# Kernel tuning notes

Measured on AMD Instinct MI355X. Metric: run time of the kernel, lower is better.

The kernel has to match this reference:

```python
import jax, jax.numpy as jnp
import numpy as np

N_NODES = 100000
N_EDGES = 800000
H = 128
MAX_Z = 1000
N_GRAPHS = 500  # batch = repeat(arange(500), 200); subgraphs are contiguous


def setup_inputs() -> dict:
    key = jax.random.key(0)
    ks = jax.random.split(key, 16)
    z = jax.random.randint(ks[0], (N_NODES,), 0, MAX_Z)
    edge_index = jax.random.randint(ks[1], (2, N_EDGES), 0, N_NODES)
    batch = jnp.repeat(jnp.arange(N_GRAPHS), N_NODES // N_GRAPHS)
    edge_mask = jax.random.randint(ks[2], (N_EDGES,), 0, 2).astype(bool)
    s = 1.0 / np.sqrt(H)
    inp = {
        "z": z, "edge_index": edge_index, "batch": batch, "edge_mask": edge_mask,
        "z_table": jax.random.normal(ks[3], (MAX_Z, H), dtype=jnp.float32) * 0.02,
        "W0": jax.random.uniform(ks[4], (H, H), minval=-s, maxval=s),
        "b0": jax.random.uniform(ks[5], (H,), minval=-s, maxval=s),
        "W1": jax.random.uniform(ks[6], (H, H), minval=-s, maxval=s),
        "b1": jax.random.uniform(ks[7], (H,), minval=-s, maxval=s),
        "W2": jax.random.uniform(ks[8], (H, H), minval=-s, maxval=s),
        "b2": jax.random.uniform(ks[9], (H,), minval=-s, maxval=s),
        "lin1_w": jax.random.uniform(ks[10], (H, H), minval=-s, maxval=s),
        "lin1_b": jax.random.uniform(ks[11], (H,), minval=-s, maxval=s),
        "lin2_w": jax.random.uniform(ks[12], (H, 1), minval=-s, maxval=s),
        "lin2_b": jax.random.uniform(ks[13], (1,), minval=-s, maxval=s),
    }
    return inp


def _gcn_conv(x, W, b, src, dst, w):
    # PyG GCNConv with self-loops (fill=1) and symmetric normalization.
    xw = x @ W                                                # [N,H]
    deg = jax.ops.segment_sum(w, dst, num_segments=N_NODES) + 1.0
    dinv = jax.lax.rsqrt(deg)                                 # deg >= 1 (self-loop)
    coef = (dinv[src] * w * dinv[dst])[:, None]               # [E,1]
    out = jax.ops.segment_sum(coef * xw[src], dst, num_segments=N_NODES)
    out = out + (dinv * dinv)[:, None] * xw                   # self-loop messages
    return out + b


def reference(z, edge_index, batch, edge_mask, z_table,
              W0, b0, W1, b1, W2, b2, lin1_w, lin1_b, lin2_w, lin2_b):
    x = z_table[z]                                            # z embedding, [N,H]
    src, dst = edge_index[0], edge_index[1]
    # fuse='minus': edge_index[:, edge_mask] == zero-weight masked-out edges
    w = edge_mask.astype(x.dtype)
    x = jax.nn.relu(_gcn_conv(x, W0, b0, src, dst, w))        # dropout: eval mode
    x = jax.nn.relu(_gcn_conv(x, W1, b1, src, dst, w))
    x = _gcn_conv(x, W2, b2, src, dst, w)
    # hadamard pooling: first two nodes of each (sorted, contiguous) subgraph
    center = jnp.searchsorted(batch, jnp.arange(N_GRAPHS))
    x = x[center] * x[center + 1]                             # [G,H]
    x = jax.nn.relu(x @ lin1_w + lin1_b)
    return x @ lin2_w + lin2_b                                # [G,1]
```

## Files before the change

kernel.cpp:

```cpp
#include <hip/hip_runtime.h>

#define N_NODES 100000
#define N_EDGES 800000
#define EHALF (N_EDGES / 2)
#define H 128
#define MAX_Z 1000
#define N_GRAPHS 500
#define ELL_CAP 32
#define NB 391
#define TB 125
#define MAXC1 33008
#define NC_ROWS 1008
#define CTR0 0
#define CTR1 64
#define LA_GRID 2080
#define LB_GRID 1040
#define N0_GRID 2064

typedef __attribute__((ext_vector_type(8))) short bf16x8;
typedef __attribute__((ext_vector_type(4))) float f32x4;

__device__ __forceinline__ unsigned short f2bf(float f) {
    union { float f; unsigned u; } x; x.f = f;
    unsigned r = x.u + 0x7fffu + ((x.u >> 16) & 1u);
    return (unsigned short)(r >> 16);
}
__device__ __forceinline__ float bf2f(unsigned short u) {
    return __uint_as_float((unsigned)u << 16);
}
__device__ __forceinline__ int clampid(int p) {
    return (p < 0 || p >= N_NODES) ? 0 : p;
}

__global__ void k_setup(int* fill, int* f0, int* f1, int* ctrs,
                        const float* W0, const float* W1, const float* W2,
                        unsigned short* Wp, const float* ztab,
                        unsigned short* tabb) {
    int b = blockIdx.x;
    if (b < NB) {
        int i = b * 256 + threadIdx.x;
        if (i < N_NODES) { fill[i] = 0; f0[i] = 0; f1[i] = 0; }
        if (i < 128) ctrs[i] = 0;
    } else if (b < NB + 24) {
        int bb = b - NB;
        int wi = bb >> 3;
        const float* W = (wi == 0) ? W0 : (wi == 1) ? W1 : W2;
        int t = (bb & 7) * 256 + threadIdx.x;
        int lane = t & 63, kt = (t >> 6) & 3, c = t >> 8;
        int quad = lane >> 4, n = c * 16 + (lane & 15);
        unsigned short o[8];
#pragma unroll
        for (int j = 0; j < 8; j++)
            o[j] = f2bf(W[(kt * 32 + quad * 8 + j) * H + n]);
        ushort4 lo = { o[0], o[1], o[2], o[3] }, hi = { o[4], o[5], o[6], o[7] };
        unsigned short* dst = Wp + (size_t)wi * 16384 + (size_t)t * 8;
        *(ushort4*)(dst)     = lo;
        *(ushort4*)(dst + 4) = hi;
    } else {
        int i = (b - NB - 24) * 256 + threadIdx.x;
        if (i < MAX_Z * H / 4) {
            float4 v = *(const float4*)(ztab + (size_t)i * 4);
            ushort4 o = { f2bf(v.x), f2bf(v.y), f2bf(v.z), f2bf(v.w) };
            *(ushort4*)(tabb + (size_t)i * 4) = o;
        }
    }
}

__global__ void k_edge(const int* __restrict__ src, const int* __restrict__ dst,
                       const int* __restrict__ mask, int* fill, int* ell) {
    int e = blockIdx.x * 256 + threadIdx.x;
    if (e >= EHALF) return;
    int m0 = mask[e], m1 = mask[e + EHALF];
    int d0 = dst[e],  d1 = dst[e + EHALF];
    int s0 = src[e],  s1 = src[e + EHALF];
    if (m0) {
        int p = atomicAdd(&fill[d0], 1);
        if (p < ELL_CAP) ell[(size_t)d0 * ELL_CAP + p] = s0;
    }
    if (m1) {
        int p = atomicAdd(&fill[d1], 1);
        if (p < ELL_CAP) ell[(size_t)d1 * ELL_CAP + p] = s1;
    }
}

__global__ void k_n1(const int* fill, const int* ell, int* f1, int* f0,
                     int* list1, int* list0, int* ctrs) {
    __shared__ int wtot[4];
    __shared__ int bbase0, bbase1;
    int tid = threadIdx.x, lane = tid & 63, wv = tid >> 6;
    int c = blockIdx.x * 4 + wv;
    int s = -1;
    if (c < 2 * N_GRAPHS) {
        int v = (c >> 1) * 200 + (c & 1);
        int n = fill[v]; if (n > ELL_CAP) n = ELL_CAP;
        s = (lane < n) ? ell[(size_t)v * ELL_CAP + lane] : ((lane == n) ? v : -1);
    }
    bool need = false;
    if (s >= 0 && atomicExch(&f1[s], 1) == 0) {
        f0[s] = 1;
        need = true;
    }
    unsigned long long b = __ballot(need);
    int total = __popcll(b);
    int pre = __popcll(b & ((1ull << lane) - 1ull));
    if (lane == 0) wtot[wv] = total;
    __syncthreads();
    if (tid == 0) {
        int bt = wtot[0] + wtot[1] + wtot[2] + wtot[3];
        if (bt) {
            bbase1 = atomicAdd(&ctrs[CTR1], bt);
            bbase0 = atomicAdd(&ctrs[CTR0], bt);
        }
    }
    __syncthreads();
    if (need) {
        int off = pre;
        for (int w2 = 0; w2 < 4; w2++) if (w2 < wv) off += wtot[w2];
        list1[bbase1 + off] = s;
        list0[bbase0 + off] = s;
    }
}

__global__ void k_n0(const int* fill, const int* ell, const int* list1,
                     int* f0, int* list0, int* ctrs) {
    __shared__ int wtot[4];
    __shared__ int bbase;
    int tid = threadIdx.x, lane = tid & 63, wv = tid >> 6;
    int cnt1 = ctrs[CTR1];
    for (int base = blockIdx.x * 4; base < cnt1; base += N0_GRID * 4) {
        int i = base + wv;
        bool need = false;
        int s = 0;
        if (i < cnt1) {
            int v = list1[i];
            int n = fill[v]; if (n > ELL_CAP) n = ELL_CAP;
            if (lane < n) {
                s = ell[(size_t)v * ELL_CAP + lane];
                need = (atomicExch(&f0[s], 1) == 0);
            }
        }
        unsigned long long b = __ballot(need);
        int total = __popcll(b);
        int pre = __popcll(b & ((1ull << lane) - 1ull));
        if (lane == 0) wtot[wv] = total;
        __syncthreads();
        if (tid == 0) {
            int bt = wtot[0] + wtot[1] + wtot[2] + wtot[3];
            if (bt) bbase = atomicAdd(&ctrs[CTR0], bt);
        }
        __syncthreads();
        if (need) {
            int off = pre;
            for (int w2 = 0; w2 < 4; w2++) if (w2 < wv) off += wtot[w2];
            list0[bbase + off] = s;
        }
        __syncthreads();
    }
}

__global__ __launch_bounds__(512) void k_layerA(const int* __restrict__ z,
                                                const unsigned short* __restrict__ tabb,
                                                const int* __restrict__ ell,
                                                const int* __restrict__ fill,
                                                const int* __restrict__ list,
                                                const int* countp,
                                                const unsigned short* __restrict__ Wp,
                                                const float* __restrict__ bias,
                                                unsigned short* xb) {
    __shared__ unsigned short yt[16][136];
    int count = *countp;
    int tid = threadIdx.x, lane = tid & 63, wv = tid >> 6;
    int l2 = lane * 2;
    int m = lane & 15, quad = lane >> 4;

    for (int t = blockIdx.x; t * 16 < count; t += LA_GRID) {
        for (int q = 0; q < 2; q++) {
            int r = t * 16 + wv * 2 + q;
            float ax = 0.f, ay = 0.f;
            if (r < count) {
                int v = list[r];
                int ntrue = fill[v];
                int px = 0;
                if (lane < ELL_CAP) px = ell[(size_t)v * ELL_CAP + lane];
                px = clampid(px);
                int zx = z[px];
                int fx = fill[px];
                int zv = z[v];
                int n = ntrue > ELL_CAP ? ELL_CAP : ntrue;
                float dv = rsqrtf(1.0f + (float)ntrue);
                float pc = (lane < n) ? rsqrtf(1.0f + (float)fx) * dv : 0.f;
                float sc = dv * dv;
                ushort2 xs = *(const ushort2*)(tabb + (size_t)zv * H + l2);
                ax = sc * bf2f(xs.x); ay = sc * bf2f(xs.y);
                int k = 0;
                for (; k + 3 < n; k += 4) {
                    int z0 = __shfl(zx, k),   z1 = __shfl(zx, k + 1);
                    int z2 = __shfl(zx, k + 2), z3 = __shfl(zx, k + 3);
                    float c0 = __shfl(pc, k),   c1 = __shfl(pc, k + 1);
                    float c2 = __shfl(pc, k + 2), c3 = __shfl(pc, k + 3);
                    ushort2 m0 = *(const ushort2*)(tabb + (size_t)z0 * H + l2);
                    ushort2 m1 = *(const ushort2*)(tabb + (size_t)z1 * H + l2);
                    ushort2 m2 = *(const ushort2*)(tabb + (size_t)z2 * H + l2);
                    ushort2 m3 = *(const ushort2*)(tabb + (size_t)z3 * H + l2);
                    ax += c0 * bf2f(m0.x) + c1 * bf2f(m1.x) + c2 * bf2f(m2.x) + c3 * bf2f(m3.x);
                    ay += c0 * bf2f(m0.y) + c1 * bf2f(m1.y) + c2 * bf2f(m2.y) + c3 * bf2f(m3.y);
                }
                for (; k < n; k++) {
                    int zz = __shfl(zx, k); float c = __shfl(pc, k);
                    ushort2 m0 = *(const ushort2*)(tabb + (size_t)zz * H + l2);
                    ax += c * bf2f(m0.x); ay += c * bf2f(m0.y);
                }
            }
            ushort2 o; o.x = f2bf(ax); o.y = f2bf(ay);
            *(ushort2*)&yt[wv * 2 + q][l2] = o;
        }
        __syncthreads();

        bf16x8 a0 = *(const bf16x8*)&yt[m][quad * 8];
        bf16x8 a1 = *(const bf16x8*)&yt[m][32 + quad * 8];
        bf16x8 a2 = *(const bf16x8*)&yt[m][64 + quad * 8];
        bf16x8 a3 = *(const bf16x8*)&yt[m][96 + quad * 8];
        const unsigned short* bp = Wp + ((size_t)(wv * 4) * 64 + lane) * 8;
        bf16x8 b0 = *(const bf16x8*)(bp);
        bf16x8 b1 = *(const bf16x8*)(bp + 64 * 8);
        bf16x8 b2 = *(const bf16x8*)(bp + 128 * 8);
        bf16x8 b3 = *(const bf16x8*)(bp + 192 * 8);
        f32x4 a = (f32x4){0.f, 0.f, 0.f, 0.f};
        a = __builtin_amdgcn_mfma_f32_16x16x32_bf16(a0, b0, a, 0, 0, 0);
        a = __builtin_amdgcn_mfma_f32_16x16x32_bf16(a1, b1, a, 0, 0, 0);
        a = __builtin_amdgcn_mfma_f32_16x16x32_bf16(a2, b2, a, 0, 0, 0);
        a = __builtin_amdgcn_mfma_f32_16x16x32_bf16(a3, b3, a, 0, 0, 0);

        int r0 = t * 16 + quad * 4;
        int col = wv * 16 + m;
        float bv = bias[col];
#pragma unroll
        for (int i = 0; i < 4; i++) {
            int r = r0 + i;
            if (r < count)
                xb[(size_t)list[r] * H + col] = f2bf(fmaxf(a[i] + bv, 0.f));
        }
        __syncthreads();
    }
}

__global__ __launch_bounds__(512) void k_layerB(const unsigned short* __restrict__ xin,
                                                const int* __restrict__ ell,
                                                const int* __restrict__ fill,
                                                const int* __restrict__ list,
                                                const int* countp,
                                                const unsigned short* __restrict__ Wp,
                                                const float* __restrict__ bias,
                                                unsigned short* xout) {
    __shared__ unsigned short yt[16][136];
    int count = *countp;
    int tid = threadIdx.x, lane = tid & 63, wv = tid >> 6;
    int l2 = lane * 2;
    int m = lane & 15, quad = lane >> 4;

    for (int t = blockIdx.x; t * 16 < count; t += LB_GRID) {
        for (int q = 0; q < 2; q++) {
            int r = t * 16 + wv * 2 + q;
            float ax = 0.f, ay = 0.f;
            if (r < count) {
                int v = list[r];
                int ntrue = fill[v];
                int px = 0;
                if (lane < ELL_CAP) px = ell[(size_t)v * ELL_CAP + lane];
                px = clampid(px);
                int fx = fill[px];
                ushort2 xs = *(const ushort2*)(xin + (size_t)v * H + l2);
                int n = ntrue > ELL_CAP ? ELL_CAP : ntrue;
                float dv = rsqrtf(1.0f + (float)ntrue);
                float pc = (lane < n) ? rsqrtf(1.0f + (float)fx) * dv : 0.f;
                float sc = dv * dv;
                ax = sc * bf2f(xs.x); ay = sc * bf2f(xs.y);
                int k = 0;
                for (; k + 3 < n; k += 4) {
                    int s0 = __shfl(px, k),   s1 = __shfl(px, k + 1);
                    int s2 = __shfl(px, k + 2), s3 = __shfl(px, k + 3);
                    float c0 = __shfl(pc, k),   c1 = __shfl(pc, k + 1);
                    float c2 = __shfl(pc, k + 2), c3 = __shfl(pc, k + 3);
                    ushort2 m0 = *(const ushort2*)(xin + (size_t)s0 * H + l2);
                    ushort2 m1 = *(const ushort2*)(xin + (size_t)s1 * H + l2);
                    ushort2 m2 = *(const ushort2*)(xin + (size_t)s2 * H + l2);
                    ushort2 m3 = *(const ushort2*)(xin + (size_t)s3 * H + l2);
                    ax += c0 * bf2f(m0.x) + c1 * bf2f(m1.x) + c2 * bf2f(m2.x) + c3 * bf2f(m3.x);
                    ay += c0 * bf2f(m0.y) + c1 * bf2f(m1.y) + c2 * bf2f(m2.y) + c3 * bf2f(m3.y);
                }
                for (; k < n; k++) {
                    int s = __shfl(px, k); float c = __shfl(pc, k);
                    ushort2 m0 = *(const ushort2*)(xin + (size_t)s * H + l2);
                    ax += c * bf2f(m0.x); ay += c * bf2f(m0.y);
                }
            }
            ushort2 o; o.x = f2bf(ax); o.y = f2bf(ay);
            *(ushort2*)&yt[wv * 2 + q][l2] = o;
        }
        __syncthreads();

        bf16x8 a0 = *(const bf16x8*)&yt[m][quad * 8];
        bf16x8 a1 = *(const bf16x8*)&yt[m][32 + quad * 8];
        bf16x8 a2 = *(const bf16x8*)&yt[m][64 + quad * 8];
        bf16x8 a3 = *(const bf16x8*)&yt[m][96 + quad * 8];
        const unsigned short* bp = Wp + ((size_t)(wv * 4) * 64 + lane) * 8;
        bf16x8 b0 = *(const bf16x8*)(bp);
        bf16x8 b1 = *(const bf16x8*)(bp + 64 * 8);
        bf16x8 b2 = *(const bf16x8*)(bp + 128 * 8);
        bf16x8 b3 = *(const bf16x8*)(bp + 192 * 8);
        f32x4 a = (f32x4){0.f, 0.f, 0.f, 0.f};
        a = __builtin_amdgcn_mfma_f32_16x16x32_bf16(a0, b0, a, 0, 0, 0);
        a = __builtin_amdgcn_mfma_f32_16x16x32_bf16(a1, b1, a, 0, 0, 0);
        a = __builtin_amdgcn_mfma_f32_16x16x32_bf16(a2, b2, a, 0, 0, 0);
        a = __builtin_amdgcn_mfma_f32_16x16x32_bf16(a3, b3, a, 0, 0, 0);

        int r0 = t * 16 + quad * 4;
        int col = wv * 16 + m;
        float bv = bias[col];
#pragma unroll
        for (int i = 0; i < 4; i++) {
            int r = r0 + i;
            if (r < count)
                xout[(size_t)list[r] * H + col] = f2bf(fmaxf(a[i] + bv, 0.f));
        }
        __syncthreads();
    }
}

__global__ __launch_bounds__(256) void k_layer2(const unsigned short* __restrict__ xin,
                                                const int* __restrict__ ell,
                                                const int* __restrict__ fill,
                                                const unsigned short* __restrict__ Wp,
                                                const float* b2,
                                                const float* l1w, const float* l1b,
                                                const float* l2w, const float* l2b,
                                                float* out) {
    __shared__ unsigned short yt[16][136];
    __shared__ float ct[16][132];
    int t = blockIdx.x;
    int tid = threadIdx.x, lane = tid & 63, wv = tid >> 6;
    int l2 = lane * 2;

    for (int q = 0; q < 4; q++) {
        int idx = t * 16 + wv * 4 + q;
        float ax = 0.f, ay = 0.f;
        if (idx < 2 * N_GRAPHS) {
            int v = (idx >> 1) * 200 + (idx & 1);
            int ntrue = fill[v];
            int px = 0;
            if (lane < ELL_CAP) px = ell[(size_t)v * ELL_CAP + lane];
            px = clampid(px);
            int fx = fill[px];
            ushort2 xs = *(const ushort2*)(xin + (size_t)v * H + l2);
            int n = ntrue > ELL_CAP ? ELL_CAP : ntrue;
            float dv = rsqrtf(1.0f + (float)ntrue);
            float pc = (lane < n) ? rsqrtf(1.0f + (float)fx) * dv : 0.f;
            float sc = dv * dv;
            ax = sc * bf2f(xs.x); ay = sc * bf2f(xs.y);
            int k = 0;
            for (; k + 3 < n; k += 4) {
                int s0 = __shfl(px, k),   s1 = __shfl(px, k + 1);
                int s2 = __shfl(px, k + 2), s3 = __shfl(px, k + 3);
                float c0 = __shfl(pc, k),   c1 = __shfl(pc, k + 1);
                float c2 = __shfl(pc, k + 2), c3 = __shfl(pc, k + 3);
                ushort2 m0 = *(const ushort2*)(xin + (size_t)s0 * H + l2);
                ushort2 m1 = *(const ushort2*)(xin + (size_t)s1 * H + l2);
                ushort2 m2 = *(const ushort2*)(xin + (size_t)s2 * H + l2);
                ushort2 m3 = *(const ushort2*)(xin + (size_t)s3 * H + l2);
                ax += c0 * bf2f(m0.x) + c1 * bf2f(m1.x) + c2 * bf2f(m2.x) + c3 * bf2f(m3.x);
                ay += c0 * bf2f(m0.y) + c1 * bf2f(m1.y) + c2 * bf2f(m2.y) + c3 * bf2f(m3.y);
            }
            for (; k < n; k++) {
                int s = __shfl(px, k); float c = __shfl(pc, k);
                ushort2 m0 = *(const ushort2*)(xin + (size_t)s * H + l2);
                ax += c * bf2f(m0.x); ay += c * bf2f(m0.y);
            }
        }
        ushort2 o; o.x = f2bf(ax); o.y = f2bf(ay);
        *(ushort2*)&yt[wv * 4 + q][l2] = o;
    }
    __syncthreads();

    int m = lane & 15, quad = lane >> 4;
    bf16x8 a0 = *(const bf16x8*)&yt[m][quad * 8];
    bf16x8 a1 = *(const bf16x8*)&yt[m][32 + quad * 8];
    bf16x8 a2 = *(const bf16x8*)&yt[m][64 + quad * 8];
    bf16x8 a3 = *(const bf16x8*)&yt[m][96 + quad * 8];

#pragma unroll
    for (int c2 = 0; c2 < 2; c2++) {
        int c = wv * 2 + c2;
        const unsigned short* bp = Wp + ((size_t)(c * 4) * 64 + lane) * 8;
        bf16x8 b0 = *(const bf16x8*)(bp);
        bf16x8 b1 = *(const bf16x8*)(bp + 64 * 8);
        bf16x8 bb = *(const bf16x8*)(bp + 128 * 8);
        bf16x8 b3 = *(const bf16x8*)(bp + 192 * 8);
        f32x4 a = (f32x4){0.f, 0.f, 0.f, 0.f};
        a = __builtin_amdgcn_mfma_f32_16x16x32_bf16(a0, b0, a, 0, 0, 0);
        a = __builtin_amdgcn_mfma_f32_16x16x32_bf16(a1, b1, a, 0, 0, 0);
        a = __builtin_amdgcn_mfma_f32_16x16x32_bf16(a2, bb, a, 0, 0, 0);
        a = __builtin_amdgcn_mfma_f32_16x16x32_bf16(a3, b3, a, 0, 0, 0);
        int col = c * 16 + m;
        float bv = b2[col];
#pragma unroll
        for (int i = 0; i < 4; i++)
            ct[quad * 4 + i][col] = a[i] + bv;
    }
    __syncthreads();

    int gl = tid >> 5, jq = tid & 31, j4 = jq * 4;
    int g = t * 8 + gl;
    float4 h = *(const float4*)(l1b + j4);
    const float* r0 = &ct[2 * gl][0];
    const float* r1 = &ct[2 * gl + 1][0];
#pragma unroll 4
    for (int k = 0; k < H; k++) {
        float pk = r0[k] * r1[k];
        float4 wv4 = *(const float4*)(l1w + (size_t)k * H + j4);
        h.x += pk * wv4.x; h.y += pk * wv4.y;
        h.z += pk * wv4.z; h.w += pk * wv4.w;
    }
    float4 l2v = *(const float4*)(l2w + j4);
    float s = fmaxf(h.x, 0.f) * l2v.x + fmaxf(h.y, 0.f) * l2v.y +
              fmaxf(h.z, 0.f) * l2v.z + fmaxf(h.w, 0.f) * l2v.w;
#pragma unroll
    for (int d = 16; d > 0; d >>= 1) s += __shfl_xor(s, d, 32);
    if (jq == 0 && g < N_GRAPHS) out[g] = s + l2b[0];
}

extern "C" void kernel_launch(void* const* d_in, const int* in_sizes, int n_in,
                              void* d_out, int out_size, void* d_ws, size_t ws_size,
                              hipStream_t stream) {
    const int*   z    = (const int*)d_in[0];
    const int*   esrc = (const int*)d_in[1];
    const int*   edst = ((const int*)d_in[1]) + N_EDGES;
    const int*   mask = (const int*)d_in[3];
    const float* ztab = (const float*)d_in[4];
    const float* W0   = (const float*)d_in[5];
    const float* b0   = (const float*)d_in[6];
    const float* W1   = (const float*)d_in[7];
    const float* b1   = (const float*)d_in[8];
    const float* W2   = (const float*)d_in[9];
    const float* b2   = (const float*)d_in[10];
    const float* l1w  = (const float*)d_in[11];
    const float* l1b  = (const float*)d_in[12];
    const float* l2w  = (const float*)d_in[13];
    const float* l2b  = (const float*)d_in[14];
    float* out = (float*)d_out;

    char* w = (char*)d_ws;
    size_t o = 0;
    auto carve = [&](size_t bytes) { char* p = w + o; o = (o + bytes + 255) & ~(size_t)255; return p; };
    unsigned short* xb    = (unsigned short*)carve((size_t)N_NODES * H * 2);
    unsigned short* xc    = (unsigned short*)carve((size_t)N_NODES * H * 2);
    int*            fill  = (int*)carve((size_t)N_NODES * 4);
    int*            ell   = (int*)carve((size_t)N_NODES * ELL_CAP * 4);
    int*            f0    = (int*)carve((size_t)N_NODES * 4);
    int*            f1    = (int*)carve((size_t)N_NODES * 4);
    int*            list0 = (int*)carve((size_t)N_NODES * 4);
    int*            list1 = (int*)carve((size_t)MAXC1 * 4);
    int*            ctrs  = (int*)carve(512);
    unsigned short* Wp    = (unsigned short*)carve((size_t)3 * 16384 * 2);
    unsigned short* tabb  = (unsigned short*)carve((size_t)MAX_Z * H * 2);

    k_setup<<<NB + 24 + TB, 256, 0, stream>>>(fill, f0, f1, ctrs,
                                              W0, W1, W2, Wp, ztab, tabb);
    k_edge <<<(EHALF + 255) / 256, 256, 0, stream>>>(esrc, edst, mask, fill, ell);
    k_n1   <<<(2 * N_GRAPHS + 3) / 4, 256, 0, stream>>>(fill, ell, f1, f0, list1, list0, ctrs);
    k_n0   <<<N0_GRID, 256, 0, stream>>>(fill, ell, list1, f0, list0, ctrs);

    k_layerA<<<LA_GRID, 512, 0, stream>>>(z, tabb, ell, fill, list0,
                                          &ctrs[CTR0], Wp, b0, xb);
    k_layerB<<<LB_GRID, 512, 0, stream>>>(xb, ell, fill, list1, &ctrs[CTR1],
                                          Wp + 16384, b1, xc);
    k_layer2<<<NC_ROWS / 16, 256, 0, stream>>>(xc, ell, fill, Wp + 32768, b2,
                                               l1w, l1b, l2w, l2b, out);
}
```

Measured before the change: 174.9 us.

## Precompute embedding-table GEMM and aggregate transformed rows in layer 0

Because the first layer's inputs are rows of the embedding table, the weight multiply is applied once to the 1000-row table (T0 = z_table @ W0) rather than to every aggregated node row. Layer 0 then becomes a pure gather-and-sum over T0 with bias and relu, with no shared-memory tile, MFMA or block barriers per 16 rows. This relies on linearity and adds one small GEMM kernel launch. Rounding changes slightly because the bf16 rounding of T0 now happens before aggregation instead of after it.

```diff
diff --git a/kernel.cpp b/kernel.cpp
--- a/kernel.cpp
+++ b/kernel.cpp
@@ -13,7 +13,7 @@
 #define NC_ROWS 1008
 #define CTR0 0
 #define CTR1 64
-#define LA_GRID 2080
+#define AG_GRID 6144
 #define LB_GRID 1040
 #define N0_GRID 2064
 
@@ -66,6 +66,37 @@
     }
 }
 
+__global__ __launch_bounds__(512) void k_tgemm(const unsigned short* __restrict__ tabb,
+                                               const unsigned short* __restrict__ Wp,
+                                               unsigned short* T0) {
+    int tid = threadIdx.x, lane = tid & 63, wv = tid >> 6;
+    int m = lane & 15, quad = lane >> 4;
+    int t = blockIdx.x;
+    int row = t * 16 + m;
+    const unsigned short* ar = tabb + (size_t)(row < MAX_Z ? row : 0) * H + quad * 8;
+    bf16x8 a0 = *(const bf16x8*)(ar);
+    bf16x8 a1 = *(const bf16x8*)(ar + 32);
+    bf16x8 a2 = *(const bf16x8*)(ar + 64);
+    bf16x8 a3 = *(const bf16x8*)(ar + 96);
+    const unsigned short* bp = Wp + ((size_t)(wv * 4) * 64 + lane) * 8;
+    bf16x8 b0 = *(const bf16x8*)(bp);
+    bf16x8 b1 = *(const bf16x8*)(bp + 64 * 8);
+    bf16x8 b2 = *(const bf16x8*)(bp + 128 * 8);
+    bf16x8 b3 = *(const bf16x8*)(bp + 192 * 8);
+    f32x4 a = (f32x4){0.f, 0.f, 0.f, 0.f};
+    a = __builtin_amdgcn_mfma_f32_16x16x32_bf16(a0, b0, a, 0, 0, 0);
+    a = __builtin_amdgcn_mfma_f32_16x16x32_bf16(a1, b1, a, 0, 0, 0);
+    a = __builtin_amdgcn_mfma_f32_16x16x32_bf16(a2, b2, a, 0, 0, 0);
+    a = __builtin_amdgcn_mfma_f32_16x16x32_bf16(a3, b3, a, 0, 0, 0);
+    int r0 = t * 16 + quad * 4;
+    int col = wv * 16 + m;
+#pragma unroll
+    for (int i = 0; i < 4; i++) {
+        int r = r0 + i;
+        if (r < MAX_Z) T0[(size_t)r * H + col] = f2bf(a[i]);
+    }
+}
+
 __global__ void k_edge(const int* __restrict__ src, const int* __restrict__ dst,
                        const int* __restrict__ mask, int* fill, int* ell) {
     int e = blockIdx.x * 256 + threadIdx.x;
@@ -158,89 +189,56 @@
     }
 }
 
-__global__ __launch_bounds__(512) void k_layerA(const int* __restrict__ z,
-                                                const unsigned short* __restrict__ tabb,
-                                                const int* __restrict__ ell,
-                                                const int* __restrict__ fill,
-                                                const int* __restrict__ list,
-                                                const int* countp,
-                                                const unsigned short* __restrict__ Wp,
-                                                const float* __restrict__ bias,
-                                                unsigned short* xb) {
-    __shared__ unsigned short yt[16][136];
+__global__ __launch_bounds__(256) void k_agg0(const int* __restrict__ z,
+                                              const unsigned short* __restrict__ T0,
+                                              const int* __restrict__ ell,
+                                              const int* __restrict__ fill,
+                                              const int* __restrict__ list,
+                                              const int* countp,
+                                              const float* __restrict__ bias,
+                                              unsigned short* xb) {
     int count = *countp;
     int tid = threadIdx.x, lane = tid & 63, wv = tid >> 6;
     int l2 = lane * 2;
-    int m = lane & 15, quad = lane >> 4;
-
-    for (int t = blockIdx.x; t * 16 < count; t += LA_GRID) {
-        for (int q = 0; q < 2; q++) {
-            int r = t * 16 + wv * 2 + q;
-            float ax = 0.f, ay = 0.f;
-            if (r < count) {
-                int v = list[r];
-                int ntrue = fill[v];
-                int px = 0;
-                if (lane < ELL_CAP) px = ell[(size_t)v * ELL_CAP + lane];
-                px = clampid(px);
-                int zx = z[px];
-                int fx = fill[px];
-                int zv = z[v];
-                int n = ntrue > ELL_CAP ? ELL_CAP : ntrue;
-                float dv = rsqrtf(1.0f + (float)ntrue);
-                float pc = (lane < n) ? rsqrtf(1.0f + (float)fx) * dv : 0.f;
-                float sc = dv * dv;
-                ushort2 xs = *(const ushort2*)(tabb + (size_t)zv * H + l2);
-                ax = sc * bf2f(xs.x); ay = sc * bf2f(xs.y);
-                int k = 0;
-                for (; k + 3 < n; k += 4) {
-                    int z0 = __shfl(zx, k),   z1 = __shfl(zx, k + 1);
-                    int z2 = __shfl(zx, k + 2), z3 = __shfl(zx, k + 3);
-                    float c0 = __shfl(pc, k),   c1 = __shfl(pc, k + 1);
-                    float c2 = __shfl(pc, k + 2), c3 = __shfl(pc, k + 3);
-                    ushort2 m0 = *(const ushort2*)(tabb + (size_t)z0 * H + l2);
-                    ushort2 m1 = *(const ushort2*)(tabb + (size_t)z1 * H + l2);
-                    ushort2 m2 = *(const ushort2*)(tabb + (size_t)z2 * H + l2);
-                    ushort2 m3 = *(const ushort2*)(tabb + (size_t)z3 * H + l2);
-                    ax += c0 * bf2f(m0.x) + c1 * bf2f(m1.x) + c2 * bf2f(m2.x) + c3 * bf2f(m3.x);
-                    ay += c0 * bf2f(m0.y) + c1 * bf2f(m1.y) + c2 * bf2f(m2.y) + c3 * bf2f(m3.y);
-                }
-                for (; k < n; k++) {
-                    int zz = __shfl(zx, k); float c = __shfl(pc, k);
-                    ushort2 m0 = *(const ushort2*)(tabb + (size_t)zz * H + l2);
-                    ax += c * bf2f(m0.x); ay += c * bf2f(m0.y);
-                }
-            }
-            ushort2 o; o.x = f2bf(ax); o.y = f2bf(ay);
-            *(ushort2*)&yt[wv * 2 + q][l2] = o;
-        }
-        __syncthreads();
-
-        bf16x8 a0 = *(const bf16x8*)&yt[m][quad * 8];
-        bf16x8 a1 = *(const bf16x8*)&yt[m][32 + quad * 8];
-        bf16x8 a2 = *(const bf16x8*)&yt[m][64 + quad * 8];
-        bf16x8 a3 = *(const bf16x8*)&yt[m][96 + quad * 8];
-        const unsigned short* bp = Wp + ((size_t)(wv * 4) * 64 + lane) * 8;
-        bf16x8 b0 = *(const bf16x8*)(bp);
-        bf16x8 b1 = *(const bf16x8*)(bp + 64 * 8);
-        bf16x8 b2 = *(const bf16x8*)(bp + 128 * 8);
-        bf16x8 b3 = *(const bf16x8*)(bp + 192 * 8);
-        f32x4 a = (f32x4){0.f, 0.f, 0.f, 0.f};
-        a = __builtin_amdgcn_mfma_f32_16x16x32_bf16(a0, b0, a, 0, 0, 0);
-        a = __builtin_amdgcn_mfma_f32_16x16x32_bf16(a1, b1, a, 0, 0, 0);
-        a = __builtin_amdgcn_mfma_f32_16x16x32_bf16(a2, b2, a, 0, 0, 0);
-        a = __builtin_amdgcn_mfma_f32_16x16x32_bf16(a3, b3, a, 0, 0, 0);
-
-        int r0 = t * 16 + quad * 4;
-        int col = wv * 16 + m;
-        float bv = bias[col];
-#pragma unroll
-        for (int i = 0; i < 4; i++) {
-            int r = r0 + i;
-            if (r < count)
-                xb[(size_t)list[r] * H + col] = f2bf(fmaxf(a[i] + bv, 0.f));
-        }
-        __syncthreads();
+    float2 bv = *(const float2*)(bias + l2);
+    for (int i = blockIdx.x * 4 + wv; i < count; i += AG_GRID * 4) {
+        int v = list[i];
+        int ntrue = fill[v];
+        int px = 0;
+        if (lane < ELL_CAP) px = ell[(size_t)v * ELL_CAP + lane];
+        px = clampid(px);
+        int zx = z[px];
+        int fx = fill[px];
+        int zv = z[v];
+        int n = ntrue > ELL_CAP ? ELL_CAP : ntrue;
+        float dv = rsqrtf(1.0f + (float)ntrue);
+        float pc = (lane < n) ? rsqrtf(1.0f + (float)fx) * dv : 0.f;
+        float sc = dv * dv;
+        ushort2 xs = *(const ushort2*)(T0 + (size_t)zv * H + l2);
+        float ax = sc * bf2f(xs.x) + bv.x;
+        float ay = sc * bf2f(xs.y) + bv.y;
+        int k = 0;
+        for (; k + 3 < n; k += 4) {
+            int z0 = __shfl(zx, k),   z1 = __shfl(zx, k + 1);
+            int z2 = __shfl(zx, k + 2), z3 = __shfl(zx, k + 3);
+            float c0 = __shfl(pc, k),   c1 = __shfl(pc, k + 1);
+            float c2 = __shfl(pc, k + 2), c3 = __shfl(pc, k + 3);
+            ushort2 m0 = *(const ushort2*)(T0 + (size_t)z0 * H + l2);
+            ushort2 m1 = *(const ushort2*)(T0 + (size_t)z1 * H + l2);
+            ushort2 m2 = *(const ushort2*)(T0 + (size_t)z2 * H + l2);
+            ushort2 m3 = *(const ushort2*)(T0 + (size_t)z3 * H + l2);
+            ax += c0 * bf2f(m0.x) + c1 * bf2f(m1.x) + c2 * bf2f(m2.x) + c3 * bf2f(m3.x);
+            ay += c0 * bf2f(m0.y) + c1 * bf2f(m1.y) + c2 * bf2f(m2.y) + c3 * bf2f(m3.y);
+        }
+        for (; k < n; k++) {
+            int zz = __shfl(zx, k); float c = __shfl(pc, k);
+            ushort2 m0 = *(const ushort2*)(T0 + (size_t)zz * H + l2);
+            ax += c * bf2f(m0.x); ay += c * bf2f(m0.y);
+        }
+        ushort2 o;
+        o.x = f2bf(fmaxf(ax, 0.f));
+        o.y = f2bf(fmaxf(ay, 0.f));
+        *(ushort2*)(xb + (size_t)v * H + l2) = o;
     }
 }
 
@@ -462,15 +460,17 @@
     int*            ctrs  = (int*)carve(512);
     unsigned short* Wp    = (unsigned short*)carve((size_t)3 * 16384 * 2);
     unsigned short* tabb  = (unsigned short*)carve((size_t)MAX_Z * H * 2);
+    unsigned short* T0    = (unsigned short*)carve((size_t)MAX_Z * H * 2);
 
     k_setup<<<NB + 24 + TB, 256, 0, stream>>>(fill, f0, f1, ctrs,
                                               W0, W1, W2, Wp, ztab, tabb);
+    k_tgemm<<<NC_ROWS / 16, 512, 0, stream>>>(tabb, Wp, T0);
     k_edge <<<(EHALF + 255) / 256, 256, 0, stream>>>(esrc, edst, mask, fill, ell);
     k_n1   <<<(2 * N_GRAPHS + 3) / 4, 256, 0, stream>>>(fill, ell, f1, f0, list1, list0, ctrs);
     k_n0   <<<N0_GRID, 256, 0, stream>>>(fill, ell, list1, f0, list0, ctrs);
 
-    k_layerA<<<LA_GRID, 512, 0, stream>>>(z, tabb, ell, fill, list0,
-                                          &ctrs[CTR0], Wp, b0, xb);
+    k_agg0<<<AG_GRID, 256, 0, stream>>>(z, T0, ell, fill, list0, &ctrs[CTR0],
+                                        b0, xb);
     k_layerB<<<LB_GRID, 512, 0, stream>>>(xb, ell, fill, list1, &ctrs[CTR1],
                                           Wp + 16384, b1, xc);
     k_layer2<<<NC_ROWS / 16, 256, 0, stream>>>(xc, ell, fill, Wp + 32768, b2,
```

After: 173.6 us. Within noise of the previous version (-0.8%).
